# Kernel tuning notes

Measured on AMD Instinct MI355X. Metric: run time of the kernel, lower is better.

The kernel has to match this reference:

```python
import jax, jax.numpy as jnp
import numpy as np

D_MODEL = 256
N_LEVELS = 4
N_HEADS = 8
N_POINTS = 4
LEN_Q = 1024
LEN_X = 256
SHAPES_NP = np.array([[100, 100], [50, 50], [25, 25], [13, 13]], dtype=np.int32)
LEN_IN = int((SHAPES_NP[:, 0] * SHAPES_NP[:, 1]).sum())  # 13294


def setup_inputs() -> dict:
    key = jax.random.key(0)
    ks = jax.random.split(key, 10)
    s = 0.02
    lvl_start = np.concatenate([[0], np.cumsum(SHAPES_NP[:, 0] * SHAPES_NP[:, 1])[:-1]]).astype(np.int32)
    return {
        "query": jax.random.normal(ks[0], (1, LEN_Q, D_MODEL), jnp.float32),
        "reference_points": jax.random.uniform(ks[1], (1, LEN_Q, N_LEVELS, 2), jnp.float32),
        "input_flatten": jax.random.normal(ks[2], (1, LEN_IN, D_MODEL), jnp.float32),
        "input_spatial_shapes": jnp.asarray(SHAPES_NP, jnp.int32),
        "add_keys": jax.random.normal(ks[3], (1, LEN_X, D_MODEL), jnp.float32),
        "input_level_start_index": jnp.asarray(lvl_start, jnp.int32),
        "W_off": jax.random.normal(ks[4], (N_HEADS * N_LEVELS * N_POINTS * 2, D_MODEL), jnp.float32) * s,
        "b_off": jax.random.normal(ks[5], (N_HEADS * N_LEVELS * N_POINTS * 2,), jnp.float32),
        "W_attn": jax.random.normal(ks[6], (N_HEADS * (N_LEVELS + 1), D_MODEL, D_MODEL), jnp.float32) * s,
        "W_val": jax.random.normal(ks[7], (2 * N_HEADS, D_MODEL, D_MODEL), jnp.float32) * s,
        "b_val": jax.random.normal(ks[8], (2 * N_HEADS, D_MODEL), jnp.float32) * s,
        "W_mix": jax.random.normal(ks[9], (D_MODEL, N_HEADS + 1), jnp.float32) * s,
    }


def reference(query, reference_points, input_flatten, input_spatial_shapes, add_keys,
              input_level_start_index, W_off, b_off, W_attn, W_val, b_val, W_mix):
    N, Lq, C = query.shape
    H, L, P = N_HEADS, N_LEVELS, N_POINTS

    # sampling offsets: (N, Lq, H, L, P, 2)
    off = (query @ W_off.T + b_off).reshape(N, Lq, H, L, P, 2)
    iss_f = input_spatial_shapes.astype(jnp.float32)          # (L, 2) = (H_l, W_l)
    wh = iss_f[:, ::-1]                                        # (W_l, H_l)
    loc = reference_points[:, :, None, :, None, :] + off / wh[None, None, None, :, None, :]

    # get_keys: clamp, quantize to int index (matches torch .int() trunc, values >= 0)
    loc = jnp.clip(loc, 0.0, 0.999)
    idx = (loc * iss_f[None, None, None, :, None, :]).astype(jnp.int32)
    h_l = input_spatial_shapes[:, 0]                           # (L,)
    flat_idx = (idx[..., 0] + idx[..., 1] * h_l[None, None, None, :, None]
                + input_level_start_index[None, None, None, :, None])   # (N, Lq, H, L, P)
    keys = input_flatten[0][flat_idx[0]]                       # (Lq, H, L, P, C)
    keys = jnp.transpose(keys, (1, 2, 3, 0, 4))                # (H, L, P, Lq, C)

    q = query.reshape(Lq, C)
    head_w = jax.nn.softmax(W_mix.T, axis=0)                   # (H+1, C), softmax over heads
    result = q * head_w[-1][None]
    addk = add_keys.reshape(-1, C)                             # (Lx, C)

    for h in range(H):
        attn = []
        for lvl in range(L):
            simil = W_attn[h * L + lvl]
            # faithful to torch: (C, P*Lq) row-major reshaped to (P, Lq, C)
            ki = (simil @ keys[h, lvl].reshape(-1, C).T).reshape(P, Lq, C)
            attn.append((ki * q[None]).sum(-1))                # (P, Lq)
        simil = W_attn[h * L + L]
        ki = addk @ simil.T                                    # (Lx, C)
        attn.append(ki @ q.T)                                  # (Lx, Lq)
        attn = jax.nn.softmax(jnp.concatenate(attn, axis=0), axis=0)  # (L*P+Lx, Lq)

        vals = (keys[h].reshape(-1, C) @ W_val[2 * h].T + b_val[2 * h]).reshape(L * P, Lq, C)
        v2 = addk @ W_val[2 * h + 1].T + b_val[2 * h + 1]      # (Lx, C)
        vals = jnp.concatenate([vals, jnp.broadcast_to(v2[:, None], (v2.shape[0], Lq, C))], axis=0)
        result = result + (attn[:, :, None] * vals).sum(0) * head_w[h][None]

    return result[None]
```

## Files before the change

kernel.cpp:

```cpp
#include <hip/hip_runtime.h>

typedef unsigned short ushort_t;
typedef __attribute__((ext_vector_type(8))) short bh8;
typedef __attribute__((ext_vector_type(4))) float f4;
typedef __attribute__((ext_vector_type(4))) unsigned int u4;

__device__ __forceinline__ ushort_t f2bf(float f) {
  unsigned u = __float_as_uint(f);
  return (ushort_t)((u + 0x7FFFu + ((u >> 16) & 1u)) >> 16);
}
__device__ __forceinline__ float bf2f(ushort_t v) {
  return __uint_as_float(((unsigned)v) << 16);
}

template <typename OutT>
__device__ __forceinline__ void gemm_abt_core(
    char* smem,
    const ushort_t* __restrict__ A, const ushort_t* __restrict__ B,
    OutT* __restrict__ C, int ldA, int ldB, int ldC, int K, int m0, int n0)
{
  ushort_t* As = (ushort_t*)smem;
  ushort_t* Bs = (ushort_t*)(smem + 10240);
  int t = threadIdx.x;
  int lane = t & 63, w = t >> 6;
  int quad = lane >> 4, l15 = lane & 15;
  int wm = w >> 1, wn = w & 1;
  f4 acc[4][4];
  #pragma unroll
  for (int mi = 0; mi < 4; ++mi)
    #pragma unroll
    for (int ni = 0; ni < 4; ++ni) acc[mi][ni] = (f4)0.f;
  int row = t >> 1, kh = (t & 1) * 16;
  const ushort_t* pa = A + (m0 + row) * ldA + kh;
  const ushort_t* pb = B + (n0 + row) * ldB + kh;
  u4 va0 = *(const u4*)(pa);     u4 va1 = *(const u4*)(pa + 8);
  u4 vb0 = *(const u4*)(pb);     u4 vb1 = *(const u4*)(pb + 8);
  for (int k0 = 0; k0 < K; k0 += 32) {
    if (k0) __syncthreads();
    {
      u4* da = (u4*)(As + row * 40 + kh); da[0] = va0; da[1] = va1;
      u4* db = (u4*)(Bs + row * 40 + kh); db[0] = vb0; db[1] = vb1;
    }
    if (k0 + 32 < K) {
      va0 = *(const u4*)(pa + k0 + 32); va1 = *(const u4*)(pa + k0 + 40);
      vb0 = *(const u4*)(pb + k0 + 32); vb1 = *(const u4*)(pb + k0 + 40);
    }
    __syncthreads();
    bh8 af[4], bfv[4];
    #pragma unroll
    for (int mi = 0; mi < 4; ++mi)
      af[mi] = *(bh8*)(As + (wm * 64 + mi * 16 + l15) * 40 + quad * 8);
    #pragma unroll
    for (int ni = 0; ni < 4; ++ni)
      bfv[ni] = *(bh8*)(Bs + (wn * 64 + ni * 16 + l15) * 40 + quad * 8);
    #pragma unroll
    for (int mi = 0; mi < 4; ++mi)
      #pragma unroll
      for (int ni = 0; ni < 4; ++ni)
        acc[mi][ni] = __builtin_amdgcn_mfma_f32_16x16x32_bf16(af[mi], bfv[ni], acc[mi][ni], 0, 0, 0);
  }
  #pragma unroll
  for (int mi = 0; mi < 4; ++mi)
    #pragma unroll
    for (int ni = 0; ni < 4; ++ni)
      #pragma unroll
      for (int r = 0; r < 4; ++r) {
        int mg = m0 + wm * 64 + mi * 16 + quad * 4 + r;
        int ng = n0 + wn * 64 + ni * 16 + l15;
        if constexpr (sizeof(OutT) == 4) C[mg * ldC + ng] = acc[mi][ni][r];
        else C[mg * ldC + ng] = (OutT)f2bf(acc[mi][ni][r]);
      }
}

__global__ __launch_bounds__(256) void k_fused_cast_off(
    const float* __restrict__ q, const float* __restrict__ xin,
    const float* __restrict__ addk, const float* __restrict__ Wval,
    const float* __restrict__ Wattn, ushort_t* __restrict__ arena,
    const float* __restrict__ Woff, float* __restrict__ off_buf)
{
  if (blockIdx.x >= 128) {
    const int total4 = 1850240;
    for (int i = (blockIdx.x - 128) * 256 + threadIdx.x; i < total4; i += 1920 * 256) {
      const float* src; ushort_t* dst; int e;
      if (i < 65536)        { src = q    + i * 4;            dst = arena + i * 4; }
      else if (i < 916352)  { e = i - 65536;  src = xin  + e * 4; dst = arena + 262144  + e * 4; }
      else if (i < 932736)  { e = i - 916352; src = addk + e * 4; dst = arena + 3665408 + e * 4; }
      else if (i < 1194880) {
        e = i - 932736; int el = e * 4;
        int h = el >> 17, r = el & 131071;
        int c = r >> 9, k = r & 511;
        src = Wval + (2 * h + (k >> 8)) * 65536 + c * 256 + (k & 255);
        dst = arena + 3730944 + el;
      }
      else if (i < 1325952) {
        e = i - 1194880; int el = e * 4;
        int h = el >> 16, off = el & 65535;
        src = Wattn + h * 262144 + 262144 + off;
        dst = arena + 5828096 + el;
      }
      else {
        e = i - 1325952;
        src = Wattn + e * 4;
        dst = arena + 6352384 + e * 4;
      }
      float4 v = *(const float4*)src;
      ushort4 o; o.x = f2bf(v.x); o.y = f2bf(v.y); o.z = f2bf(v.z); o.w = f2bf(v.w);
      *(ushort4*)dst = o;
    }
  } else {
    __shared__ float As[16][65];
    __shared__ float Bs[16][65];
    int e = blockIdx.x;
    int kh2 = e >> 6; e &= 63;
    int nx = e & 3, my = e >> 2;
    int m0 = my * 64, n0 = nx * 64;
    int kbase = kh2 * 128;
    int t = threadIdx.x;
    int tm = t & 15, tn = t >> 4;
    int lr = t >> 4, lc = t & 15;
    float acc[4][4] = {};
    float qa[4], wb[4];
    #pragma unroll
    for (int i = 0; i < 4; ++i) {
      int r = lr + i * 16;
      qa[i] = q[(m0 + r) * 256 + kbase + lc];
      wb[i] = Woff[(n0 + r) * 256 + kbase + lc];
    }
    for (int k0 = kbase; k0 < kbase + 128; k0 += 16) {
      if (k0 != kbase) __syncthreads();
      #pragma unroll
      for (int i = 0; i < 4; ++i) {
        int r = lr + i * 16;
        As[lc][r] = qa[i];
        Bs[lc][r] = wb[i];
      }
      if (k0 + 16 < kbase + 128) {
        #pragma unroll
        for (int i = 0; i < 4; ++i) {
          int r = lr + i * 16;
          qa[i] = q[(m0 + r) * 256 + k0 + 16 + lc];
          wb[i] = Woff[(n0 + r) * 256 + k0 + 16 + lc];
        }
      }
      __syncthreads();
      #pragma unroll
      for (int k = 0; k < 16; ++k) {
        float a[4], b[4];
        #pragma unroll
        for (int i = 0; i < 4; ++i) a[i] = As[k][tm * 4 + i];
        #pragma unroll
        for (int j = 0; j < 4; ++j) b[j] = Bs[k][tn * 4 + j];
        #pragma unroll
        for (int i = 0; i < 4; ++i)
          #pragma unroll
          for (int j = 0; j < 4; ++j) acc[i][j] += a[i] * b[j];
      }
    }
    #pragma unroll
    for (int i = 0; i < 4; ++i)
      #pragma unroll
      for (int j = 0; j < 4; ++j)
        off_buf[kh2 * 262144 + (m0 + tm * 4 + i) * 256 + n0 + tn * 4 + j] = acc[i][j];
  }
}

__global__ __launch_bounds__(256) void k_fused_idx_g4(
    const float* __restrict__ off_buf, const float* __restrict__ boff,
    const float* __restrict__ refpts, const int* __restrict__ shapes,
    const int* __restrict__ lvlst, int* __restrict__ fidx,
    const ushort_t* __restrict__ addk, const ushort_t* __restrict__ Wattn4,
    ushort_t* __restrict__ tmp)
{
  __shared__ __align__(16) char smem[20480];
  if (blockIdx.x >= 32) {
    int t = threadIdx.x;
    int b = (blockIdx.x - 32) * 2 + (t >> 7), tt = t & 127;
    int l = (tt >> 2) & 3;
    float off0 = off_buf[b * 256 + 2 * tt]     + off_buf[262144 + b * 256 + 2 * tt]     + boff[2 * tt];
    float off1 = off_buf[b * 256 + 2 * tt + 1] + off_buf[262144 + b * 256 + 2 * tt + 1] + boff[2 * tt + 1];
    int Hi = shapes[2 * l], Wi = shapes[2 * l + 1];
    float Hf = (float)Hi, Wf = (float)Wi;
    float r0 = refpts[b * 8 + 2 * l], r1 = refpts[b * 8 + 2 * l + 1];
    float l0 = fminf(fmaxf(r0 + off0 / Wf, 0.f), 0.999f);
    float l1 = fminf(fmaxf(r1 + off1 / Hf, 0.f), 0.999f);
    int i0 = (int)(l0 * Hf);
    int i1 = (int)(l1 * Wf);
    fidx[b * 128 + tt] = i0 + i1 * Hi + lvlst[l];
  } else {
    int e = blockIdx.x;
    int h = e >> 2, rem = e & 3, my = rem >> 1, nx = rem & 1;
    gemm_abt_core<ushort_t>(smem, addk, Wattn4 + h * 65536, tmp + h * 65536,
                            256, 256, 256, 256, my * 128, nx * 128);
  }
}

__device__ __forceinline__ void attn_mfma_body(
    char* smemc,
    const ushort_t* __restrict__ qbf, const ushort_t* __restrict__ xbf,
    const ushort_t* __restrict__ Wlvl, const int* __restrict__ fidx,
    float* __restrict__ attnP, int bx)
{
  unsigned* Bs = (unsigned*)smemc;
  ushort_t* As = (ushort_t*)(smemc + 8704);
  int* fis = (int*)(smemc + 17920);
  float* Nlds = (float*)smemc;

  int h = bx >> 8, l = (bx >> 6) & 3, g = bx & 63;
  int ch = g & 3, g2 = g >> 2;
  int p = g2 >> 2, tg = g2 & 3;
  int c0 = ch * 64;
  int t = threadIdx.x;
  int lane = t & 63, w = t >> 6;
  int quad = lane >> 4, l15 = lane & 15;
  int qcol = p * 4 + tg;
  fis[t] = fidx[(tg * 256 + t) * 128 + h * 16 + l * 4 + p];
  __syncthreads();
  f4 acc[4];
  #pragma unroll
  for (int mi = 0; mi < 4; ++mi) acc[mi] = (f4)0.f;

  int cl = t & 63, sg = t >> 6;
  int uu = t >> 2, jj0 = (t & 3) * 16;
  const ushort_t* qrow = qbf + (uu * 16 + qcol) * 256 + jj0;

  unsigned vv[16];
  u4 a0, a1;
  #pragma unroll
  for (int rr = 0; rr < 16; ++rr)
    vv[rr] = xbf[fis[sg * 16 + rr] * 256 + c0 + cl];
  { const u4* src = (const u4*)qrow; a0 = src[0]; a1 = src[1]; }

  #pragma unroll
  for (int jt = 0; jt < 4; ++jt) {
    if (jt) __syncthreads();
    #pragma unroll
    for (int i = 0; i < 4; ++i) {
      uint2 w2; w2.x = vv[i * 4] | (vv[i * 4 + 1] << 16);
      w2.y = vv[i * 4 + 2] | (vv[i * 4 + 3] << 16);
      *(uint2*)&Bs[cl * 34 + sg * 8 + i * 2] = w2;
    }
    { u4* dst = (u4*)(As + uu * 72 + jj0); dst[0] = a0; dst[1] = a1; }
    if (jt < 3) {
      #pragma unroll
      for (int rr = 0; rr < 16; ++rr)
        vv[rr] = xbf[fis[(jt + 1) * 64 + sg * 16 + rr] * 256 + c0 + cl];
      const u4* src = (const u4*)(qrow + (jt + 1) * 64);
      a0 = src[0]; a1 = src[1];
    }
    __syncthreads();
    #pragma unroll
    for (int ks = 0; ks < 2; ++ks) {
      bh8 af[4], bfv;
      #pragma unroll
      for (int mi = 0; mi < 4; ++mi)
        af[mi] = *(bh8*)(As + (mi * 16 + l15) * 72 + ks * 32 + quad * 8);
      {
        const unsigned* bp = &Bs[(w * 16 + l15) * 34 + ks * 16 + quad * 4];
        uint2 b0 = *(const uint2*)bp;
        uint2 b1 = *(const uint2*)(bp + 2);
        u4 bb; bb.x = b0.x; bb.y = b0.y; bb.z = b1.x; bb.w = b1.y;
        bfv = __builtin_bit_cast(bh8, bb);
      }
      #pragma unroll
      for (int mi = 0; mi < 4; ++mi)
        acc[mi] = __builtin_amdgcn_mfma_f32_16x16x32_bf16(af[mi], bfv, acc[mi], 0, 0, 0);
    }
  }
  __syncthreads();
  #pragma unroll
  for (int mi = 0; mi < 4; ++mi)
    *(f4*)&Nlds[(w * 16 + l15) * 68 + mi * 16 + quad * 4] = acc[mi];
  __syncthreads();
  {
    int a = t >> 6, u = t & 63;
    const ushort_t* Wr = Wlvl + (h * 4 + l) * 65536 + (a * 64 + u) * 256 + c0;
    float s = 0.f;
    #pragma unroll
    for (int cc = 0; cc < 8; ++cc) {
      u4 wv = *(const u4*)(Wr + cc * 8);
      int cb = cc * 8;
      s += __uint_as_float(wv.x << 16)         * Nlds[(cb + 0) * 68 + u];
      s += __uint_as_float(wv.x & 0xffff0000u) * Nlds[(cb + 1) * 68 + u];
      s += __uint_as_float(wv.y << 16)         * Nlds[(cb + 2) * 68 + u];
      s += __uint_as_float(wv.y & 0xffff0000u) * Nlds[(cb + 3) * 68 + u];
      s += __uint_as_float(wv.z << 16)         * Nlds[(cb + 4) * 68 + u];
      s += __uint_as_float(wv.z & 0xffff0000u) * Nlds[(cb + 5) * 68 + u];
      s += __uint_as_float(wv.w << 16)         * Nlds[(cb + 6) * 68 + u];
      s += __uint_as_float(wv.w & 0xffff0000u) * Nlds[(cb + 7) * 68 + u];
    }
    attnP[ch * 131072 + (h * 16 + l * 4 + a) * 1024 + u * 16 + qcol] = s;
  }
}

__global__ __launch_bounds__(256) void k_fused_attn(
    const ushort_t* __restrict__ qbf, const ushort_t* __restrict__ xbf,
    const ushort_t* __restrict__ Wlvl, const int* __restrict__ fidx,
    float* __restrict__ attnP,
    const ushort_t* __restrict__ tmp, float* __restrict__ attn)
{
  __shared__ __align__(16) char smem[20480];
  int bx = blockIdx.x;
  if (bx >= 128) {
    attn_mfma_body(smem, qbf, xbf, Wlvl, fidx, attnP, bx - 128);
  } else {
    int e = bx;
    int h = e >> 4, rem = e & 15, my = rem >> 3, nx = rem & 7;
    gemm_abt_core<float>(smem, tmp + h * 65536, qbf, attn + h * 278528 + 16384,
                         256, 256, 1024, 256, my * 128, nx * 128);
  }
}

__global__ __launch_bounds__(256) void k_softmax(
    float* __restrict__ attn, const float* __restrict__ attnP,
    ushort_t* __restrict__ attn2bf, float* __restrict__ s1, float* __restrict__ s2)
{
  __shared__ float red[16][17];
  int h = blockIdx.y;
  int bl = threadIdx.x & 15;
  int b = blockIdx.x * 16 + bl;
  int rg = threadIdx.x >> 4;
  const int R0 = rg * 17;
  float* col = attn + h * 278528 + b;
  float v[17];
  float m = -1e30f;
  #pragma unroll
  for (int i = 0; i < 17; ++i) {
    int r = R0 + i;
    float x;
    if (r < 16) {
      int idx = (h * 16 + r) * 1024 + b;
      x = attnP[idx] + attnP[131072 + idx] + attnP[262144 + idx] + attnP[393216 + idx];
    } else {
      x = col[r * 1024];
    }
    v[i] = x;
    m = fmaxf(m, x);
  }
  red[rg][bl] = m;
  __syncthreads();
  #pragma unroll
  for (int j = 0; j < 16; ++j) m = fmaxf(m, red[j][bl]);
  float sum = 0.f;
  #pragma unroll
  for (int i = 0; i < 17; ++i) { v[i] = expf(v[i] - m); sum += v[i]; }
  __syncthreads();
  red[rg][bl] = sum;
  __syncthreads();
  float tot = 0.f;
  #pragma unroll
  for (int j = 0; j < 16; ++j) tot += red[j][bl];
  float inv = 1.f / tot;
  #pragma unroll
  for (int i = 0; i < 17; ++i) {
    int r = R0 + i;
    float x = v[i] * inv;
    if (r < 16) col[r * 1024] = x;
    else attn2bf[h * 262144 + (r - 16) * 1024 + b] = f2bf(x);
  }
  if (rg == 0) {
    float sa = 0.f;
    #pragma unroll
    for (int i = 0; i < 16; ++i) sa += v[i];
    float sn = sa * inv;
    s1[h * 1024 + b] = sn;
    s2[h * 1024 + b] = 1.f - sn;
  }
}

__global__ __launch_bounds__(256) void k_fused_kbar_tn(
    const ushort_t* __restrict__ xbf, const float* __restrict__ attn,
    const int* __restrict__ fidx, const ushort_t* __restrict__ attn2,
    const ushort_t* __restrict__ addk, ushort_t* __restrict__ kabar)
{
  __shared__ __align__(16) unsigned Asu[128 * 20];
  __shared__ __align__(16) unsigned Bsu[128 * 20];
  if (blockIdx.x >= 128) {
    int bb = blockIdx.x - 128;
    int h = bb >> 7, b0 = (bb & 127) * 8;
    int t = threadIdx.x;
    int qi = t >> 5, oct = t & 31;
    int b = b0 + qi;
    float aw[16]; int rowv[16];
    #pragma unroll
    for (int r = 0; r < 16; ++r) {
      aw[r]   = attn[(h * 272 + r) * 1024 + b];
      rowv[r] = fidx[b * 128 + h * 16 + r];
    }
    u4 va[8], vb[8];
    #pragma unroll
    for (int r = 0; r < 8; ++r) va[r] = *(const u4*)(xbf + rowv[r] * 256 + oct * 8);
    #pragma unroll
    for (int r = 0; r < 8; ++r) vb[r] = *(const u4*)(xbf + rowv[8 + r] * 256 + oct * 8);
    float sacc[8] = {};
    #pragma unroll
    for (int r = 0; r < 8; ++r) {
      u4 v = va[r]; float w = aw[r];
      sacc[0] += w * __uint_as_float(v.x << 16);
      sacc[1] += w * __uint_as_float(v.x & 0xffff0000u);
      sacc[2] += w * __uint_as_float(v.y << 16);
      sacc[3] += w * __uint_as_float(v.y & 0xffff0000u);
      sacc[4] += w * __uint_as_float(v.z << 16);
      sacc[5] += w * __uint_as_float(v.z & 0xffff0000u);
      sacc[6] += w * __uint_as_float(v.w << 16);
      sacc[7] += w * __uint_as_float(v.w & 0xffff0000u);
    }
    #pragma unroll
    for (int r = 0; r < 8; ++r) {
      u4 v = vb[r]; float w = aw[8 + r];
      sacc[0] += w * __uint_as_float(v.x << 16);
      sacc[1] += w * __uint_as_float(v.x & 0xffff0000u);
      sacc[2] += w * __uint_as_float(v.y << 16);
      sacc[3] += w * __uint_as_float(v.y & 0xffff0000u);
      sacc[4] += w * __uint_as_float(v.z << 16);
      sacc[5] += w * __uint_as_float(v.z & 0xffff0000u);
      sacc[6] += w * __uint_as_float(v.w << 16);
      sacc[7] += w * __uint_as_float(v.w & 0xffff0000u);
    }
    u4 o;
    o.x = (unsigned)f2bf(sacc[0]) | ((unsigned)f2bf(sacc[1]) << 16);
    o.y = (unsigned)f2bf(sacc[2]) | ((unsigned)f2bf(sacc[3]) << 16);
    o.z = (unsigned)f2bf(sacc[4]) | ((unsigned)f2bf(sacc[5]) << 16);
    o.w = (unsigned)f2bf(sacc[6]) | ((unsigned)f2bf(sacc[7]) << 16);
    *(u4*)(kabar + (h * 1024 + b) * 512 + oct * 8) = o;
  } else {
    int e = blockIdx.x;
    int h = e >> 4, rem = e & 15, my = rem >> 1, nx = rem & 1;
    const ushort_t* A = attn2 + h * 262144;
    const ushort_t* B = addk;
    ushort_t* C = kabar + h * 524288;
    int m0 = my * 128, n0 = nx * 128;
    int t = threadIdx.x;
    int lane = t & 63, w = t >> 6;
    int quad = lane >> 4, l15 = lane & 15;
    int wm = w >> 1, wn = w & 1;
    f4 acc[4][4];
    #pragma unroll
    for (int mi = 0; mi < 4; ++mi)
      #pragma unroll
      for (int ni = 0; ni < 4; ++ni) acc[mi][ni] = (f4)0.f;
    int col = t & 127, half = t >> 7;
    unsigned pa[8], pb[8];
    #pragma unroll
    for (int i = 0; i < 4; ++i) {
      int kpp = half * 4 + i, kk = kpp * 4;
      unsigned x0 = A[(kk + 0) * 1024 + m0 + col], x1 = A[(kk + 1) * 1024 + m0 + col];
      unsigned x2 = A[(kk + 2) * 1024 + m0 + col], x3 = A[(kk + 3) * 1024 + m0 + col];
      pa[i * 2] = x0 | (x1 << 16); pa[i * 2 + 1] = x2 | (x3 << 16);
      unsigned y0 = B[(kk + 0) * 256 + n0 + col], y1 = B[(kk + 1) * 256 + n0 + col];
      unsigned y2 = B[(kk + 2) * 256 + n0 + col], y3 = B[(kk + 3) * 256 + n0 + col];
      pb[i * 2] = y0 | (y1 << 16); pb[i * 2 + 1] = y2 | (y3 << 16);
    }
    for (int k0 = 0; k0 < 256; k0 += 32) {
      if (k0) __syncthreads();
      #pragma unroll
      for (int i = 0; i < 4; ++i) {
        int kpp = half * 4 + i;
        uint2 va; va.x = pa[i * 2]; va.y = pa[i * 2 + 1];
        *(uint2*)&Asu[col * 20 + kpp * 2] = va;
        uint2 vbv; vbv.x = pb[i * 2]; vbv.y = pb[i * 2 + 1];
        *(uint2*)&Bsu[col * 20 + kpp * 2] = vbv;
      }
      if (k0 + 32 < 256) {
        #pragma unroll
        for (int i = 0; i < 4; ++i) {
          int kpp = half * 4 + i, kk = k0 + 32 + kpp * 4;
          unsigned x0 = A[(kk + 0) * 1024 + m0 + col], x1 = A[(kk + 1) * 1024 + m0 + col];
          unsigned x2 = A[(kk + 2) * 1024 + m0 + col], x3 = A[(kk + 3) * 1024 + m0 + col];
          pa[i * 2] = x0 | (x1 << 16); pa[i * 2 + 1] = x2 | (x3 << 16);
          unsigned y0 = B[(kk + 0) * 256 + n0 + col], y1 = B[(kk + 1) * 256 + n0 + col];
          unsigned y2 = B[(kk + 2) * 256 + n0 + col], y3 = B[(kk + 3) * 256 + n0 + col];
          pb[i * 2] = y0 | (y1 << 16); pb[i * 2 + 1] = y2 | (y3 << 16);
        }
      }
      __syncthreads();
      bh8 af[4], bfv[4];
      #pragma unroll
      for (int mi = 0; mi < 4; ++mi)
        af[mi] = *(bh8*)((const ushort_t*)Asu + (wm * 64 + mi * 16 + l15) * 40 + quad * 8);
      #pragma unroll
      for (int ni = 0; ni < 4; ++ni)
        bfv[ni] = *(bh8*)((const ushort_t*)Bsu + (wn * 64 + ni * 16 + l15) * 40 + quad * 8);
      #pragma unroll
      for (int mi = 0; mi < 4; ++mi)
        #pragma unroll
        for (int ni = 0; ni < 4; ++ni)
          acc[mi][ni] = __builtin_amdgcn_mfma_f32_16x16x32_bf16(af[mi], bfv[ni], acc[mi][ni], 0, 0, 0);
    }
    #pragma unroll
    for (int mi = 0; mi < 4; ++mi)
      #pragma unroll
      for (int ni = 0; ni < 4; ++ni)
        #pragma unroll
        for (int r = 0; r < 4; ++r) {
          int mg = m0 + wm * 64 + mi * 16 + quad * 4 + r;
          int ng = n0 + wn * 64 + ni * 16 + l15;
          C[mg * 512 + 256 + ng] = f2bf(acc[mi][ni][r]);
        }
  }
}

__global__ __launch_bounds__(256) void gemm_val_k(
    const ushort_t* __restrict__ kabar, const ushort_t* __restrict__ Wcat,
    float* __restrict__ Y, float* __restrict__ Y2)
{
  __shared__ __align__(16) char smem[20480];
  int h = blockIdx.z & 7, ks = blockIdx.z >> 3;
  float* C = (ks ? Y2 : Y) + h * 262144;
  gemm_abt_core<float>(smem, kabar + h * 524288 + ks * 256,
                       Wcat + h * 131072 + ks * 256, C,
                       512, 512, 256, 256, blockIdx.y * 128, blockIdx.x * 128);
}

__global__ __launch_bounds__(256) void k_combine(
    const float* __restrict__ q, const float* __restrict__ Wmix,
    const float* __restrict__ Y, const float* __restrict__ Y2,
    const float* __restrict__ s1, const float* __restrict__ s2,
    const float* __restrict__ bval, float* __restrict__ out)
{
  int b = blockIdx.x, c = threadIdx.x;
  float w[9];
  float m = -1e30f;
  #pragma unroll
  for (int j = 0; j < 9; ++j) { w[j] = Wmix[c * 9 + j]; m = fmaxf(m, w[j]); }
  float tot = 0.f;
  #pragma unroll
  for (int j = 0; j < 9; ++j) { w[j] = expf(w[j] - m); tot += w[j]; }
  float inv = 1.f / tot;
  float res = q[b * 256 + c] * w[8] * inv;
  #pragma unroll
  for (int hh = 0; hh < 8; ++hh) {
    int yi = (hh * 1024 + b) * 256 + c;
    float y = Y[yi] + Y2[yi]
            + s1[hh * 1024 + b] * bval[(2 * hh) * 256 + c]
            + s2[hh * 1024 + b] * bval[(2 * hh + 1) * 256 + c];
    res += w[hh] * inv * y;
  }
  out[b * 256 + c] = res;
}

extern "C" void kernel_launch(void* const* d_in, const int* in_sizes, int n_in,
                              void* d_out, int out_size, void* d_ws, size_t ws_size,
                              hipStream_t stream) {
  (void)in_sizes; (void)n_in; (void)out_size; (void)ws_size;
  const float* q      = (const float*)d_in[0];
  const float* refpts = (const float*)d_in[1];
  const float* xin    = (const float*)d_in[2];
  const int*   shapes = (const int*)d_in[3];
  const float* addk   = (const float*)d_in[4];
  const int*   lvlst  = (const int*)d_in[5];
  const float* Woff   = (const float*)d_in[6];
  const float* boff   = (const float*)d_in[7];
  const float* Wattn  = (const float*)d_in[8];
  const float* Wval   = (const float*)d_in[9];
  const float* bval   = (const float*)d_in[10];
  const float* Wmix   = (const float*)d_in[11];
  float* out = (float*)d_out;
  float* ws  = (float*)d_ws;

  int*   fidx    = (int*)ws;
  float* s1      = ws + 393216;
  float* s2      = ws + 401408;
  float* attn    = ws + 409600;
  float* Y       = ws + 409600;
  ushort_t* arena = (ushort_t*)(ws + 2637824);
  ushort_t* q_bf     = arena;
  ushort_t* xin_bf   = arena + 262144;
  ushort_t* addk_bf  = arena + 3665408;
  ushort_t* Wcat_bf  = arena + 3730944;
  ushort_t* Wattn4_bf= arena + 5828096;
  ushort_t* Wlvl_bf  = arena + 6352384;
  ushort_t* tmp_bf   = arena + 8449536;
  ushort_t* attn2_bf = arena + 8973824;
  ushort_t* kabar_bf = arena + 11070976;
  float* attnP = (float*)(arena + 15265280);
  float* off_buf = (float*)(arena + 16313856);
  float* Y2 = (float*)(arena + 17362944);

  k_fused_cast_off<<<2048, 256, 0, stream>>>(q, xin, addk, Wval, Wattn, arena,
                                             Woff, off_buf);
  k_fused_idx_g4<<<544, 256, 0, stream>>>(off_buf, boff, refpts, shapes, lvlst,
                                          fidx, addk_bf, Wattn4_bf, tmp_bf);
  k_fused_attn<<<2176, 256, 0, stream>>>(q_bf, xin_bf, Wlvl_bf, fidx, attnP,
                                         tmp_bf, attn);
  k_softmax<<<dim3(64, 8), 256, 0, stream>>>(attn, attnP, attn2_bf, s1, s2);
  k_fused_kbar_tn<<<1152, 256, 0, stream>>>(xin_bf, attn, fidx, attn2_bf,
                                            addk_bf, kabar_bf);
  gemm_val_k<<<dim3(2, 8, 16), 256, 0, stream>>>(kabar_bf, Wcat_bf, Y, Y2);
  k_combine<<<1024, 256, 0, stream>>>(q, Wmix, Y, Y2, s1, s2, bval, out);
}
```

Before: 177.8 us.

## Fold offset GEMM, index computation and add-key GEMM into the cast kernel

The offset projection now runs with the full K=256 per block and computes sampling indices in its epilogue, which removes the split-K off_buf round trip. The add-key attention GEMM moves into the first kernel and reads fp32 inputs directly, converting to bf16 while staging into shared memory, so the separate Wattn4 cast and the k_fused_idx_g4 launch disappear. The value GEMM also drops its split-K into Y/Y2 and accumulates K=512 in one pass, so k_combine reads a single buffer. In exchange there are fewer blocks for the offset and value GEMMs, which means less parallelism and longer per-block serial K loops.

```diff
diff --git a/kernel.cpp b/kernel.cpp
--- a/kernel.cpp
+++ b/kernel.cpp
@@ -72,15 +72,92 @@
       }
 }
 
+__device__ __forceinline__ void gemm_abt_f32in(
+    char* smem,
+    const float* __restrict__ A, const float* __restrict__ B,
+    ushort_t* __restrict__ C, int ldA, int ldB, int ldC, int K, int m0, int n0)
+{
+  ushort_t* As = (ushort_t*)smem;
+  ushort_t* Bs = (ushort_t*)(smem + 10240);
+  int t = threadIdx.x;
+  int lane = t & 63, w = t >> 6;
+  int quad = lane >> 4, l15 = lane & 15;
+  int wm = w >> 1, wn = w & 1;
+  f4 acc[4][4];
+  #pragma unroll
+  for (int mi = 0; mi < 4; ++mi)
+    #pragma unroll
+    for (int ni = 0; ni < 4; ++ni) acc[mi][ni] = (f4)0.f;
+  int row = t >> 1, kh = (t & 1) * 16;
+  const float* pa = A + (m0 + row) * ldA + kh;
+  const float* pb = B + (n0 + row) * ldB + kh;
+  float4 fa[4], fb[4];
+  #pragma unroll
+  for (int i = 0; i < 4; ++i) {
+    fa[i] = *(const float4*)(pa + i * 4);
+    fb[i] = *(const float4*)(pb + i * 4);
+  }
+  for (int k0 = 0; k0 < K; k0 += 32) {
+    if (k0) __syncthreads();
+    {
+      ushort_t* da = As + row * 40 + kh;
+      ushort_t* db = Bs + row * 40 + kh;
+      #pragma unroll
+      for (int i = 0; i < 4; ++i) {
+        ushort4 oa; oa.x = f2bf(fa[i].x); oa.y = f2bf(fa[i].y);
+        oa.z = f2bf(fa[i].z); oa.w = f2bf(fa[i].w);
+        *(ushort4*)(da + i * 4) = oa;
+        ushort4 ob; ob.x = f2bf(fb[i].x); ob.y = f2bf(fb[i].y);
+        ob.z = f2bf(fb[i].z); ob.w = f2bf(fb[i].w);
+        *(ushort4*)(db + i * 4) = ob;
+      }
+    }
+    if (k0 + 32 < K) {
+      #pragma unroll
+      for (int i = 0; i < 4; ++i) {
+        fa[i] = *(const float4*)(pa + k0 + 32 + i * 4);
+        fb[i] = *(const float4*)(pb + k0 + 32 + i * 4);
+      }
+    }
+    __syncthreads();
+    bh8 af[4], bfv[4];
+    #pragma unroll
+    for (int mi = 0; mi < 4; ++mi)
+      af[mi] = *(bh8*)(As + (wm * 64 + mi * 16 + l15) * 40 + quad * 8);
+    #pragma unroll
+    for (int ni = 0; ni < 4; ++ni)
+      bfv[ni] = *(bh8*)(Bs + (wn * 64 + ni * 16 + l15) * 40 + quad * 8);
+    #pragma unroll
+    for (int mi = 0; mi < 4; ++mi)
+      #pragma unroll
+      for (int ni = 0; ni < 4; ++ni)
+        acc[mi][ni] = __builtin_amdgcn_mfma_f32_16x16x32_bf16(af[mi], bfv[ni], acc[mi][ni], 0, 0, 0);
+  }
+  #pragma unroll
+  for (int mi = 0; mi < 4; ++mi)
+    #pragma unroll
+    for (int ni = 0; ni < 4; ++ni)
+      #pragma unroll
+      for (int r = 0; r < 4; ++r) {
+        int mg = m0 + wm * 64 + mi * 16 + quad * 4 + r;
+        int ng = n0 + wn * 64 + ni * 16 + l15;
+        C[mg * ldC + ng] = (ushort_t)f2bf(acc[mi][ni][r]);
+      }
+}
+
 __global__ __launch_bounds__(256) void k_fused_cast_off(
     const float* __restrict__ q, const float* __restrict__ xin,
     const float* __restrict__ addk, const float* __restrict__ Wval,
     const float* __restrict__ Wattn, ushort_t* __restrict__ arena,
-    const float* __restrict__ Woff, float* __restrict__ off_buf)
-{
-  if (blockIdx.x >= 128) {
-    const int total4 = 1850240;
-    for (int i = (blockIdx.x - 128) * 256 + threadIdx.x; i < total4; i += 1920 * 256) {
+    const float* __restrict__ Woff, const float* __restrict__ boff,
+    const float* __restrict__ refpts, const int* __restrict__ shapes,
+    const int* __restrict__ lvlst, int* __restrict__ fidx,
+    ushort_t* __restrict__ tmp)
+{
+  __shared__ __align__(16) char smem[20480];
+  if (blockIdx.x >= 96) {
+    const int total4 = 1719168;
+    for (int i = (blockIdx.x - 96) * 256 + threadIdx.x; i < total4; i += 1952 * 256) {
       const float* src; ushort_t* dst; int e;
       if (i < 65536)        { src = q    + i * 4;            dst = arena + i * 4; }
       else if (i < 916352)  { e = i - 65536;  src = xin  + e * 4; dst = arena + 262144  + e * 4; }
@@ -92,14 +169,8 @@
         src = Wval + (2 * h + (k >> 8)) * 65536 + c * 256 + (k & 255);
         dst = arena + 3730944 + el;
       }
-      else if (i < 1325952) {
-        e = i - 1194880; int el = e * 4;
-        int h = el >> 16, off = el & 65535;
-        src = Wattn + h * 262144 + 262144 + off;
-        dst = arena + 5828096 + el;
-      }
       else {
-        e = i - 1325952;
+        e = i - 1194880;
         src = Wattn + e * 4;
         dst = arena + 6352384 + e * 4;
       }
@@ -107,14 +178,17 @@
       ushort4 o; o.x = f2bf(v.x); o.y = f2bf(v.y); o.z = f2bf(v.z); o.w = f2bf(v.w);
       *(ushort4*)dst = o;
     }
+  } else if (blockIdx.x >= 64) {
+    int e = blockIdx.x - 64;
+    int h = e >> 2, rem = e & 3, my = rem >> 1, nx = rem & 1;
+    gemm_abt_f32in(smem, addk, Wattn + (h * 4 + 4) * 65536, tmp + h * 65536,
+                   256, 256, 256, 256, my * 128, nx * 128);
   } else {
-    __shared__ float As[16][65];
-    __shared__ float Bs[16][65];
+    float(*As)[65] = (float(*)[65])smem;
+    float(*Bs)[65] = (float(*)[65])(smem + 16 * 65 * 4);
     int e = blockIdx.x;
-    int kh2 = e >> 6; e &= 63;
     int nx = e & 3, my = e >> 2;
     int m0 = my * 64, n0 = nx * 64;
-    int kbase = kh2 * 128;
     int t = threadIdx.x;
     int tm = t & 15, tn = t >> 4;
     int lr = t >> 4, lc = t & 15;
@@ -123,18 +197,18 @@
     #pragma unroll
     for (int i = 0; i < 4; ++i) {
       int r = lr + i * 16;
-      qa[i] = q[(m0 + r) * 256 + kbase + lc];
-      wb[i] = Woff[(n0 + r) * 256 + kbase + lc];
-    }
-    for (int k0 = kbase; k0 < kbase + 128; k0 += 16) {
-      if (k0 != kbase) __syncthreads();
+      qa[i] = q[(m0 + r) * 256 + lc];
+      wb[i] = Woff[(n0 + r) * 256 + lc];
+    }
+    for (int k0 = 0; k0 < 256; k0 += 16) {
+      if (k0) __syncthreads();
       #pragma unroll
       for (int i = 0; i < 4; ++i) {
         int r = lr + i * 16;
         As[lc][r] = qa[i];
         Bs[lc][r] = wb[i];
       }
-      if (k0 + 16 < kbase + 128) {
+      if (k0 + 16 < 256) {
         #pragma unroll
         for (int i = 0; i < 4; ++i) {
           int r = lr + i * 16;
@@ -157,40 +231,24 @@
       }
     }
     #pragma unroll
-    for (int i = 0; i < 4; ++i)
-      #pragma unroll
-      for (int j = 0; j < 4; ++j)
-        off_buf[kh2 * 262144 + (m0 + tm * 4 + i) * 256 + n0 + tn * 4 + j] = acc[i][j];
-  }
-}
-
-__global__ __launch_bounds__(256) void k_fused_idx_g4(
-    const float* __restrict__ off_buf, const float* __restrict__ boff,
-    const float* __restrict__ refpts, const int* __restrict__ shapes,
-    const int* __restrict__ lvlst, int* __restrict__ fidx,
-    const ushort_t* __restrict__ addk, const ushort_t* __restrict__ Wattn4,
-    ushort_t* __restrict__ tmp)
-{
-  __shared__ __align__(16) char smem[20480];
-  if (blockIdx.x >= 32) {
-    int t = threadIdx.x;
-    int b = (blockIdx.x - 32) * 2 + (t >> 7), tt = t & 127;
-    int l = (tt >> 2) & 3;
-    float off0 = off_buf[b * 256 + 2 * tt]     + off_buf[262144 + b * 256 + 2 * tt]     + boff[2 * tt];
-    float off1 = off_buf[b * 256 + 2 * tt + 1] + off_buf[262144 + b * 256 + 2 * tt + 1] + boff[2 * tt + 1];
-    int Hi = shapes[2 * l], Wi = shapes[2 * l + 1];
-    float Hf = (float)Hi, Wf = (float)Wi;
-    float r0 = refpts[b * 8 + 2 * l], r1 = refpts[b * 8 + 2 * l + 1];
-    float l0 = fminf(fmaxf(r0 + off0 / Wf, 0.f), 0.999f);
-    float l1 = fminf(fmaxf(r1 + off1 / Hf, 0.f), 0.999f);
-    int i0 = (int)(l0 * Hf);
-    int i1 = (int)(l1 * Wf);
-    fidx[b * 128 + tt] = i0 + i1 * Hi + lvlst[l];
-  } else {
-    int e = blockIdx.x;
-    int h = e >> 2, rem = e & 3, my = rem >> 1, nx = rem & 1;
-    gemm_abt_core<ushort_t>(smem, addk, Wattn4 + h * 65536, tmp + h * 65536,
-                            256, 256, 256, 256, my * 128, nx * 128);
+    for (int i = 0; i < 4; ++i) {
+      int b = m0 + tm * 4 + i;
+      #pragma unroll
+      for (int jp = 0; jp < 2; ++jp) {
+        int tt = ((n0 + tn * 4) >> 1) + jp;
+        int l = (tt >> 2) & 3;
+        float off0 = acc[i][jp * 2]     + boff[2 * tt];
+        float off1 = acc[i][jp * 2 + 1] + boff[2 * tt + 1];
+        int Hi = shapes[2 * l], Wi = shapes[2 * l + 1];
+        float Hf = (float)Hi, Wf = (float)Wi;
+        float r0 = refpts[b * 8 + 2 * l], r1 = refpts[b * 8 + 2 * l + 1];
+        float l0 = fminf(fmaxf(r0 + off0 / Wf, 0.f), 0.999f);
+        float l1 = fminf(fmaxf(r1 + off1 / Hf, 0.f), 0.999f);
+        int i0 = (int)(l0 * Hf);
+        int i1 = (int)(l1 * Wf);
+        fidx[b * 128 + tt] = i0 + i1 * Hi + lvlst[l];
+      }
+    }
   }
 }
 
@@ -501,19 +559,17 @@
 
 __global__ __launch_bounds__(256) void gemm_val_k(
     const ushort_t* __restrict__ kabar, const ushort_t* __restrict__ Wcat,
-    float* __restrict__ Y, float* __restrict__ Y2)
+    float* __restrict__ Y)
 {
   __shared__ __align__(16) char smem[20480];
-  int h = blockIdx.z & 7, ks = blockIdx.z >> 3;
-  float* C = (ks ? Y2 : Y) + h * 262144;
-  gemm_abt_core<float>(smem, kabar + h * 524288 + ks * 256,
-                       Wcat + h * 131072 + ks * 256, C,
-                       512, 512, 256, 256, blockIdx.y * 128, blockIdx.x * 128);
+  int h = blockIdx.z;
+  gemm_abt_core<float>(smem, kabar + h * 524288, Wcat + h * 131072, Y + h * 262144,
+                       512, 512, 256, 512, blockIdx.y * 128, blockIdx.x * 128);
 }
 
 __global__ __launch_bounds__(256) void k_combine(
     const float* __restrict__ q, const float* __restrict__ Wmix,
-    const float* __restrict__ Y, const float* __restrict__ Y2,
+    const float* __restrict__ Y,
     const float* __restrict__ s1, const float* __restrict__ s2,
     const float* __restrict__ bval, float* __restrict__ out)
 {
@@ -529,8 +585,7 @@
   float res = q[b * 256 + c] * w[8] * inv;
   #pragma unroll
   for (int hh = 0; hh < 8; ++hh) {
-    int yi = (hh * 1024 + b) * 256 + c;
-    float y = Y[yi] + Y2[yi]
+    float y = Y[(hh * 1024 + b) * 256 + c]
             + s1[hh * 1024 + b] * bval[(2 * hh) * 256 + c]
             + s2[hh * 1024 + b] * bval[(2 * hh + 1) * 256 + c];
     res += w[hh] * inv * y;
@@ -567,24 +622,20 @@
   ushort_t* xin_bf   = arena + 262144;
   ushort_t* addk_bf  = arena + 3665408;
   ushort_t* Wcat_bf  = arena + 3730944;
-  ushort_t* Wattn4_bf= arena + 5828096;
   ushort_t* Wlvl_bf  = arena + 6352384;
   ushort_t* tmp_bf   = arena + 8449536;
   ushort_t* attn2_bf = arena + 8973824;
   ushort_t* kabar_bf = arena + 11070976;
   float* attnP = (float*)(arena + 15265280);
-  float* off_buf = (float*)(arena + 16313856);
-  float* Y2 = (float*)(arena + 17362944);
 
   k_fused_cast_off<<<2048, 256, 0, stream>>>(q, xin, addk, Wval, Wattn, arena,
-                                             Woff, off_buf);
-  k_fused_idx_g4<<<544, 256, 0, stream>>>(off_buf, boff, refpts, shapes, lvlst,
-                                          fidx, addk_bf, Wattn4_bf, tmp_bf);
+                                             Woff, boff, refpts, shapes, lvlst,
+                                             fidx, tmp_bf);
   k_fused_attn<<<2176, 256, 0, stream>>>(q_bf, xin_bf, Wlvl_bf, fidx, attnP,
                                          tmp_bf, attn);
   k_softmax<<<dim3(64, 8), 256, 0, stream>>>(attn, attnP, attn2_bf, s1, s2);
   k_fused_kbar_tn<<<1152, 256, 0, stream>>>(xin_bf, attn, fidx, attn2_bf,
                                             addk_bf, kabar_bf);
-  gemm_val_k<<<dim3(2, 8, 16), 256, 0, stream>>>(kabar_bf, Wcat_bf, Y, Y2);
-  k_combine<<<1024, 256, 0, stream>>>(q, Wmix, Y, Y2, s1, s2, bval, out);
-}
+  gemm_val_k<<<dim3(2, 8, 8), 256, 0, stream>>>(kabar_bf, Wcat_bf, Y);
+  k_combine<<<1024, 256, 0, stream>>>(q, Wmix, Y, s1, s2, bval, out);
+}
```

Result: no change. 178.5 us (+0.4%).
